# Kernel tuning notes

Hardware: AMD Instinct MI355X
Metric: run time of the kernel (lower is better)

The kernel has to match this reference:

```python
import jax, jax.numpy as jnp
import numpy as np
from jax import lax

NAG = 3          # hardcoded in the torch module (query slices, catted_torches)
B = 4096         # batch_size per agent
H = 128          # hidden_dim
HEADS = 8
AD = H // HEADS  # attend_dim
STATE, ACT, SCAN = 48, 2, 256
OUTF, HID = 10, 256
NFEAT = 32 * (SCAN - 6)  # conv output features (two VALID convs: k5 then k3)
EPS = 1e-5

def leaky(x):
    return jnp.where(x >= 0, x, 0.01 * x)

def setup_inputs() -> dict:
    key = jax.random.key(0)
    ks = iter(jax.random.split(key, 40))
    def rn(shape, scale=0.05):
        return jax.random.normal(next(ks), shape, dtype=jnp.float32) * scale
    return {
        'obs':  jax.random.normal(next(ks), (NAG * B, STATE), jnp.float32),
        'acts': jax.random.normal(next(ks), (NAG * B, ACT), jnp.float32),
        'scan': jax.random.normal(next(ks), (NAG * B, SCAN), jnp.float32),
        'conv_w1': rn((32, 1, 5)),  'conv_b1': jnp.zeros((32,), jnp.float32),
        'conv_w2': rn((32, 32, 3)), 'conv_b2': jnp.zeros((32,), jnp.float32),
        'fc_w1': rn((256, NFEAT), 0.01), 'fc_b1': jnp.zeros((256,), jnp.float32),
        'fc_w2': rn((OUTF, 256)),        'fc_b2': jnp.zeros((OUTF,), jnp.float32),
        'enc_w': rn((H, STATE + ACT + OUTF)), 'enc_b': jnp.zeros((H,), jnp.float32),
        'Wk': rn((HEADS, AD, H)),
        'Wv': rn((HEADS, AD, H)), 'bv': jnp.zeros((HEADS, AD), jnp.float32),
        'Wq': rn((NAG, HEADS, AD, H)),
        'q1_w1': rn((HID, 2 * H)), 'q1_b1': jnp.zeros((HID,), jnp.float32),
        'q1_w2': rn((HID, HID)),   'q1_b2': jnp.zeros((HID,), jnp.float32),
        'q1_w3': rn((1, HID)),     'q1_b3': jnp.zeros((1,), jnp.float32),
        'q2_w1': rn((HID, 2 * H)), 'q2_b1': jnp.zeros((HID,), jnp.float32),
        'q2_w2': rn((HID, HID)),   'q2_b2': jnp.zeros((HID,), jnp.float32),
        'q2_w3': rn((1, HID)),     'q2_b3': jnp.zeros((1,), jnp.float32),
    }

def reference(obs, acts, scan, conv_w1, conv_b1, conv_w2, conv_b2,
              fc_w1, fc_b1, fc_w2, fc_b2, enc_w, enc_b, Wk, Wv, bv, Wq,
              q1_w1, q1_b1, q1_w2, q1_b2, q1_w3, q1_b3,
              q2_w1, q2_b1, q2_w2, q2_b2, q2_w3, q2_b3):
    dn = ('NCH', 'OIH', 'NCH')
    x = scan[:, None, :]                                            # [N,1,L]
    x = lax.conv_general_dilated(x, conv_w1, (1,), 'VALID', dimension_numbers=dn)
    x = jax.nn.relu(x + conv_b1[None, :, None])
    x = lax.conv_general_dilated(x, conv_w2, (1,), 'VALID', dimension_numbers=dn)
    x = jax.nn.relu(x + conv_b2[None, :, None])
    x = x.reshape(x.shape[0], -1)                                   # [N, NFEAT]
    x = jax.nn.relu(x @ fc_w1.T + fc_b1)
    feats = x @ fc_w2.T + fc_b2                                     # [N, OUTF]

    inps = jnp.concatenate([obs, acts, feats], axis=1)
    mu, var = inps.mean(0), inps.var(0)                             # BatchNorm1d (train, no affine)
    normed = (inps - mu) / jnp.sqrt(var + EPS)
    sa = leaky(normed @ enc_w.T + enc_b).reshape(NAG, B, H)         # [ag,B,H]

    keys = jnp.einsum('gbh,ndh->ngbd', sa, Wk)                      # [hd,ag,B,ad]
    vals = leaky(jnp.einsum('gbh,ndh->ngbd', sa, Wv) + bv[:, None, None, :])
    q = jnp.einsum('gbh,gndh->gnbd', sa, Wq)                        # [ag,hd,B,ad]

    logits = jnp.einsum('gnbd,nobd->gnbo', q, keys) / np.sqrt(AD)   # [ag,hd,B,ag]
    self_mask = jnp.eye(NAG, dtype=bool)[:, None, None, :]          # exclude own agent
    logits = jnp.where(self_mask, -jnp.inf, logits)
    w = jax.nn.softmax(logits, axis=-1)
    other = jnp.einsum('gnbo,nobd->gnbd', w, vals)                  # [ag,hd,B,ad]
    other = other.transpose(0, 2, 1, 3).reshape(NAG, B, H)          # heads concatenated

    emb = jnp.concatenate([sa, other], axis=2).reshape(NAG * B, 2 * H)

    def mlp(x, w1, b1, w2, b2, w3, b3):
        x = jax.nn.relu(x @ w1.T + b1)
        x = jax.nn.relu(x @ w2.T + b2)
        return x @ w3.T + b3

    q1 = mlp(emb, q1_w1, q1_b1, q1_w2, q1_b2, q1_w3, q1_b3)
    q2 = mlp(emb, q2_w1, q2_b1, q2_w2, q2_b2, q2_w3, q2_b3)
    return (q1, q2)
```

## Files before the change

### kernel.cpp

```cpp
#include <hip/hip_runtime.h>
#include <hip/hip_bf16.h>
#include <cstdint>
#include <cstddef>

typedef unsigned short u16;
typedef __attribute__((ext_vector_type(8))) __bf16 bf16x8;
typedef __attribute__((ext_vector_type(4))) float f32x4;

__device__ __forceinline__ u16 f2b(float f) {
  __hip_bfloat16 h = __float2bfloat16(f);
  return *reinterpret_cast<u16*>(&h);
}
__device__ __forceinline__ float b2f(u16 u) {
  union { float f; uint32_t i; } x; x.i = ((uint32_t)u) << 16; return x.f;
}
__device__ __forceinline__ f32x4 mfma16(bf16x8 a, bf16x8 b, f32x4 c) {
  return __builtin_amdgcn_mfma_f32_16x16x32_bf16(a, b, c, 0, 0, 0);
}
__device__ __forceinline__ void async16(const void* g, void* l) {
  __builtin_amdgcn_global_load_lds((const __attribute__((address_space(1))) uint32_t*)g,
                                   (__attribute__((address_space(3))) uint32_t*)l, 16, 0, 0);
}

__global__ __launch_bounds__(256) void w1_perm(const float* __restrict__ w,
                                               u16* __restrict__ o) {
  __shared__ float L[8000];
  int j = blockIdx.x, tid = threadIdx.x;
  for (int i = tid; i < 8000; i += 256) L[i] = w[(size_t)j * 8000 + i];
  __syncthreads();
  for (int i = tid; i < 8000; i += 256) {
    int tt = i >> 5, c2 = i & 31;
    o[(size_t)j * 8000 + i] = f2b(L[c2 * 250 + tt]);
  }
}

struct CvtArgs {
  const float* src[7];
  u16* dst[7];
  int cum[8];
};
__global__ __launch_bounds__(256) void f2b_multi(CvtArgs a, float* stats) {
  int i = blockIdx.x * 256 + threadIdx.x;
  if (blockIdx.x == 0 && threadIdx.x < 128) stats[threadIdx.x] = 0.f;
  int seg = 0;
  #pragma unroll
  for (int s = 1; s < 7; ++s) if (i >= a.cum[s]) seg = s;
  if (i < a.cum[7]) {
    int off = i - a.cum[seg];
    a.dst[seg][off] = f2b(a.src[seg][off]);
  }
}

__global__ __launch_bounds__(256) void conv_fused(
    const float* __restrict__ scan, const float* __restrict__ cw1,
    const float* __restrict__ cb1, const float* __restrict__ cw2,
    const float* __restrict__ cb2, u16* __restrict__ x, int row0) {
  __shared__ float s[256];
  __shared__ __align__(16) u16 h1T[258 * 32];
  __shared__ __align__(16) u16 w2r[32 * 96];
  int tid = threadIdx.x;
  int lrow = blockIdx.x;
  s[tid] = scan[(size_t)(row0 + lrow) * 256 + tid];
  for (int i = tid; i < 3072; i += 256) {
    int c2 = i / 96, rem = i - c2 * 96, k = rem >> 5, c1 = rem & 31;
    w2r[i] = f2b(cw2[(c2 * 32 + c1) * 3 + k]);
  }
  if (tid < 192) h1T[252 * 32 + tid] = 0;
  __syncthreads();
  {
    int c1 = tid & 31, pb = tid >> 5;
    float w0 = cw1[c1 * 5 + 0], w1v = cw1[c1 * 5 + 1], w2v = cw1[c1 * 5 + 2],
          w3v = cw1[c1 * 5 + 3], w4v = cw1[c1 * 5 + 4];
    float bb = cb1[c1];
    int p0 = pb * 32;
    #pragma unroll 4
    for (int i = 0; i < 32; ++i) {
      int p = p0 + i;
      if (p < 252) {
        float a = bb + s[p] * w0 + s[p + 1] * w1v + s[p + 2] * w2v +
                  s[p + 3] * w3v + s[p + 4] * w4v;
        h1T[p * 32 + c1] = f2b(fmaxf(a, 0.f));
      }
    }
  }
  __syncthreads();
  int lane = tid & 63, wv = tid >> 6;
  int l15 = lane & 15, quad = lane >> 4;
  f32x4 zero = {0.f, 0.f, 0.f, 0.f};
  f32x4 acc[4][2];
  #pragma unroll
  for (int i = 0; i < 4; ++i) { acc[i][0] = zero; acc[i][1] = zero; }
  #pragma unroll
  for (int kk = 0; kk < 3; ++kk) {
    bf16x8 b0 = *(const bf16x8*)&w2r[l15 * 96 + kk * 32 + quad * 8];
    bf16x8 b1 = *(const bf16x8*)&w2r[(16 + l15) * 96 + kk * 32 + quad * 8];
    #pragma unroll
    for (int i = 0; i < 4; ++i) {
      int t = (wv * 4 + i) * 16 + l15 + kk;
      bf16x8 a = *(const bf16x8*)&h1T[t * 32 + quad * 8];
      acc[i][0] = mfma16(a, b0, acc[i][0]);
      acc[i][1] = mfma16(a, b1, acc[i][1]);
    }
  }
  float bias0 = cb2[l15], bias1 = cb2[16 + l15];
  u16* xr = x + (size_t)lrow * 8000;
  #pragma unroll
  for (int i = 0; i < 4; ++i) {
    int tb = (wv * 4 + i) * 16 + quad * 4;
    #pragma unroll
    for (int r = 0; r < 4; ++r) {
      int t = tb + r;
      if (t < 250) {
        xr[t * 32 + l15]      = f2b(fmaxf(acc[i][0][r] + bias0, 0.f));
        xr[t * 32 + 16 + l15] = f2b(fmaxf(acc[i][1][r] + bias1, 0.f));
      }
    }
  }
}

template <int MODE>
__global__ __launch_bounds__(256) void gemm_bt(
    const u16* __restrict__ A, int lda, const u16* __restrict__ W,
    const float* __restrict__ bias, float* __restrict__ outF,
    u16* __restrict__ outB, int ldo, int ksteps, int wq_sel, size_t out_zoff) {
  __shared__ __align__(16) u16 As[128 * 32];
  __shared__ __align__(16) u16 Bs[128 * 32];
  int tid = threadIdx.x;
  int m0 = blockIdx.y * 128, n0 = blockIdx.x * 128;
  if (wq_sel) W += (size_t)(blockIdx.y >> 5) * wq_sel;
  int kbase = blockIdx.z * ksteps * 32;
  if (MODE == 0) outF += (size_t)blockIdx.z * out_zoff;
  const u16* Ap = A + (size_t)m0 * lda + kbase;
  const u16* Wp = W + (size_t)n0 * lda + kbase;
  int lane = tid & 63, wv = tid >> 6;
  int l15 = lane & 15, quad = lane >> 4;
  int wm = (wv >> 1) * 64, wn = (wv & 1) * 64;
  int r0 = tid >> 2, kc = (tid & 3) * 8;
  int r1 = (tid + 256) >> 2;
  f32x4 zero = {0.f, 0.f, 0.f, 0.f};
  f32x4 acc[4][4];
  #pragma unroll
  for (int i = 0; i < 4; ++i)
    #pragma unroll
    for (int j = 0; j < 4; ++j) acc[i][j] = zero;
  for (int ks = 0; ks < ksteps; ++ks) {
    __syncthreads();
    async16(Ap + (size_t)r0 * lda + kc, &As[tid * 8]);
    async16(Wp + (size_t)r0 * lda + kc, &Bs[tid * 8]);
    async16(Ap + (size_t)r1 * lda + kc, &As[(tid + 256) * 8]);
    async16(Wp + (size_t)r1 * lda + kc, &Bs[(tid + 256) * 8]);
    __syncthreads();
    bf16x8 af[4], bfr[4];
    #pragma unroll
    for (int i = 0; i < 4; ++i)
      af[i] = *(const bf16x8*)&As[(wm + i * 16 + l15) * 32 + quad * 8];
    #pragma unroll
    for (int j = 0; j < 4; ++j)
      bfr[j] = *(const bf16x8*)&Bs[(wn + j * 16 + l15) * 32 + quad * 8];
    #pragma unroll
    for (int i = 0; i < 4; ++i)
      #pragma unroll
      for (int j = 0; j < 4; ++j) acc[i][j] = mfma16(af[i], bfr[j], acc[i][j]);
    Ap += 32; Wp += 32;
  }
  #pragma unroll
  for (int i = 0; i < 4; ++i) {
    int mb = m0 + wm + i * 16 + quad * 4;
    #pragma unroll
    for (int j = 0; j < 4; ++j) {
      int n = n0 + wn + j * 16 + l15;
      float bv_ = (MODE == 1 || MODE == 2) ? bias[n] : 0.f;
      #pragma unroll
      for (int r = 0; r < 4; ++r) {
        float v = acc[i][j][r];
        if (MODE == 0) {
          outF[(size_t)(mb + r) * ldo + n] = v;
        } else {
          v += bv_;
          if (MODE == 1) v = fmaxf(v, 0.f);
          if (MODE == 2) v = v >= 0.f ? v : 0.01f * v;
          outB[(size_t)(mb + r) * ldo + n] = f2b(v);
        }
      }
    }
  }
}

__global__ __launch_bounds__(256) void fc2_stats(
    const float* __restrict__ hparts, const float* __restrict__ b1,
    const float* __restrict__ w2, const float* __restrict__ b2,
    const float* __restrict__ obs, const float* __restrict__ acts,
    float* __restrict__ inps, float* __restrict__ stats) {
  __shared__ float hL[32 * 260];
  __shared__ float w2L[10 * 260];
  __shared__ float b1L[256];
  __shared__ float ipL[32 * 61];
  int tid = threadIdx.x, r0 = blockIdx.x * 32;
  b1L[tid] = b1[tid];
  for (int i = tid; i < 2560; i += 256) w2L[(i >> 8) * 260 + (i & 255)] = w2[i];
  for (int i = tid; i < 32 * 48; i += 256) {
    int r = i / 48, f = i - r * 48;
    ipL[r * 61 + f] = obs[(size_t)(r0 + r) * 48 + f];
  }
  if (tid < 64) {
    int r = tid >> 1, f = tid & 1;
    ipL[r * 61 + 48 + f] = acts[(size_t)(r0 + r) * 2 + f];
  }
  __syncthreads();
  const size_t HS = (size_t)12288 * 256;
  for (int i = tid; i < 32 * 256; i += 256) {
    int r = i >> 8, c = i & 255;
    size_t g = (size_t)(r0 + r) * 256 + c;
    float v = b1L[c] + hparts[g] + hparts[g + HS] + hparts[g + 2 * HS] +
              hparts[g + 3 * HS] + hparts[g + 4 * HS];
    hL[r * 260 + c] = fmaxf(v, 0.f);
  }
  __syncthreads();
  {
    int r = tid >> 3, ob = tid & 7;
    for (int o = ob; o < 10; o += 8) {
      float a = 0.f;
      #pragma unroll 8
      for (int c = 0; c < 256; ++c) a += hL[r * 260 + c] * w2L[o * 260 + c];
      ipL[r * 61 + 50 + o] = a + b2[o];
    }
  }
  __syncthreads();
  for (int i = tid; i < 32 * 60; i += 256) {
    int r = i / 60, f = i - r * 60;
    inps[(size_t)(r0 + r) * 64 + f] = ipL[r * 61 + f];
  }
  if (tid < 60) {
    float s = 0.f, s2 = 0.f;
    for (int r = 0; r < 32; ++r) {
      float v = ipL[r * 61 + tid];
      s += v; s2 += v * v;
    }
    atomicAdd(&stats[tid], s);
    atomicAdd(&stats[64 + tid], s2);
  }
}

__global__ __launch_bounds__(256) void enc_kernel(
    const float* __restrict__ inps, const float* __restrict__ stats,
    const float* __restrict__ enc_w, const float* __restrict__ enc_b,
    u16* __restrict__ sab) {
  __shared__ float ewL[128 * 61];
  __shared__ float nrm[32 * 61];
  __shared__ float ebL[128];
  __shared__ float muL[60], ivL[60];
  int tid = threadIdx.x, r0 = blockIdx.x * 32;
  if (tid < 128) ebL[tid] = enc_b[tid];
  if (tid < 60) {
    float s = stats[tid], s2 = stats[64 + tid];
    float mu = s * (1.f / 12288.f);
    float var = s2 * (1.f / 12288.f) - mu * mu;
    muL[tid] = mu;
    ivL[tid] = rsqrtf(var + 1e-5f);
  }
  for (int i = tid; i < 128 * 60; i += 256) {
    int h = i / 60, f = i - h * 60;
    ewL[h * 61 + f] = enc_w[i];
  }
  __syncthreads();
  for (int i = tid; i < 32 * 60; i += 256) {
    int r = i / 60, f = i - r * 60;
    nrm[r * 61 + f] = (inps[(size_t)(r0 + r) * 64 + f] - muL[f]) * ivL[f];
  }
  __syncthreads();
  for (int i = tid; i < 32 * 128; i += 256) {
    int r = i >> 7, h = i & 127;
    float a = ebL[h];
    #pragma unroll 4
    for (int f = 0; f < 60; ++f) a += nrm[r * 61 + f] * ewL[h * 61 + f];
    a = a >= 0.f ? a : 0.01f * a;
    sab[(size_t)(r0 + r) * 128 + h] = f2b(a);
  }
}

__global__ __launch_bounds__(128) void attn_combine(
    const u16* __restrict__ qb, const u16* __restrict__ keysb,
    const u16* __restrict__ valsb, const u16* __restrict__ sab,
    u16* __restrict__ emb) {
  __shared__ float qL[3][128], kL[3][128], vL[3][128];
  __shared__ float lg[3][8][3], wgt[3][8][3];
  int b = blockIdx.x, t = threadIdx.x;
  #pragma unroll
  for (int o = 0; o < 3; ++o) {
    size_t base = (size_t)(o * 4096 + b) * 128 + t;
    qL[o][t] = b2f(qb[base]);
    kL[o][t] = b2f(keysb[base]);
    vL[o][t] = b2f(valsb[base]);
  }
  __syncthreads();
  if (t < 72) {
    int g = t / 24, n = (t / 3) % 8, o = t % 3;
    float a = 0.f;
    #pragma unroll
    for (int d = 0; d < 16; ++d) a += qL[g][n * 16 + d] * kL[o][n * 16 + d];
    lg[g][n][o] = (o == g) ? -1e30f : a * 0.25f;
  }
  __syncthreads();
  if (t < 24) {
    int g = t / 8, n = t % 8;
    float m = fmaxf(fmaxf(lg[g][n][0], lg[g][n][1]), lg[g][n][2]);
    float e0 = expf(lg[g][n][0] - m), e1 = expf(lg[g][n][1] - m),
          e2 = expf(lg[g][n][2] - m);
    float inv = 1.f / (e0 + e1 + e2);
    wgt[g][n][0] = e0 * inv; wgt[g][n][1] = e1 * inv; wgt[g][n][2] = e2 * inv;
  }
  __syncthreads();
  int n = t >> 4, d = t & 15;
  #pragma unroll
  for (int g = 0; g < 3; ++g) {
    float o_ = wgt[g][n][0] * vL[0][n * 16 + d] +
               wgt[g][n][1] * vL[1][n * 16 + d] +
               wgt[g][n][2] * vL[2][n * 16 + d];
    size_t rbase = (size_t)(g * 4096 + b) * 256;
    emb[rbase + 128 + t] = f2b(o_);
    emb[rbase + t] = sab[(size_t)(g * 4096 + b) * 128 + t];
  }
}

__global__ __launch_bounds__(256) void final_dot(
    const u16* __restrict__ t2a, const u16* __restrict__ t2b,
    const float* __restrict__ w3a, const float* __restrict__ b3a,
    const float* __restrict__ w3b, const float* __restrict__ b3b,
    float* __restrict__ out) {
  int wv = threadIdx.x >> 6, lane = threadIdx.x & 63;
  int row = blockIdx.x * 4 + wv;
  float sa_ = 0.f, sb_ = 0.f;
  #pragma unroll
  for (int e = 0; e < 4; ++e) {
    int c = lane * 4 + e;
    sa_ += b2f(t2a[(size_t)row * 256 + c]) * w3a[c];
    sb_ += b2f(t2b[(size_t)row * 256 + c]) * w3b[c];
  }
  #pragma unroll
  for (int off = 32; off; off >>= 1) {
    sa_ += __shfl_down(sa_, off);
    sb_ += __shfl_down(sb_, off);
  }
  if (lane == 0) {
    out[row] = sa_ + b3a[0];
    out[12288 + row] = sb_ + b3b[0];
  }
}

extern "C" void kernel_launch(void* const* d_in, const int* in_sizes, int n_in,
                              void* d_out, int out_size, void* d_ws,
                              size_t ws_size, hipStream_t stream) {
  const float* obs  = (const float*)d_in[0];
  const float* acts = (const float*)d_in[1];
  const float* scan = (const float*)d_in[2];
  const float* cw1  = (const float*)d_in[3];
  const float* cb1  = (const float*)d_in[4];
  const float* cw2  = (const float*)d_in[5];
  const float* cb2  = (const float*)d_in[6];
  const float* fw1  = (const float*)d_in[7];
  const float* fb1  = (const float*)d_in[8];
  const float* fw2  = (const float*)d_in[9];
  const float* fb2  = (const float*)d_in[10];
  const float* encw = (const float*)d_in[11];
  const float* encb = (const float*)d_in[12];
  const float* Wk   = (const float*)d_in[13];
  const float* Wv   = (const float*)d_in[14];
  const float* bv   = (const float*)d_in[15];
  const float* Wq   = (const float*)d_in[16];
  const float* q1w1 = (const float*)d_in[17];
  const float* q1b1 = (const float*)d_in[18];
  const float* q1w2 = (const float*)d_in[19];
  const float* q1b2 = (const float*)d_in[20];
  const float* q1w3 = (const float*)d_in[21];
  const float* q1b3 = (const float*)d_in[22];
  const float* q2w1 = (const float*)d_in[23];
  const float* q2b1 = (const float*)d_in[24];
  const float* q2w2 = (const float*)d_in[25];
  const float* q2b2 = (const float*)d_in[26];
  const float* q2w3 = (const float*)d_in[27];
  const float* q2b3 = (const float*)d_in[28];
  float* out = (float*)d_out;
  char* ws = (char*)d_ws;
  if (ws_size < 166003712u) return;

  u16*   x     = (u16*)(ws + 0);
  u16*   w1b   = (u16*)(ws + 98304000);
  float* hpart = (float*)(ws + 102400000);
  float* stats = (float*)(ws + 165314560);
  u16*   wkb   = (u16*)(ws + 165315584);
  u16*   wvb   = (u16*)(ws + 165348352);
  u16*   wqb   = (u16*)(ws + 165381120);
  u16*   m1a   = (u16*)(ws + 165479424);
  u16*   m2a   = (u16*)(ws + 165610496);
  u16*   m1b   = (u16*)(ws + 165741568);
  u16*   m2b   = (u16*)(ws + 165872640);
  float* inps  = (float*)(ws + 0);
  u16*   sab   = (u16*)(ws + 3145728);
  u16*   keysb = (u16*)(ws + 6291456);
  u16*   valsb = (u16*)(ws + 9437184);
  u16*   qb    = (u16*)(ws + 12582912);
  u16*   embb  = (u16*)(ws + 15728640);
  u16*   t1a   = (u16*)(ws + 22020096);
  u16*   t2a   = (u16*)(ws + 28311552);
  u16*   t1b   = (u16*)(ws + 34603008);
  u16*   t2b   = (u16*)(ws + 40894464);

  w1_perm<<<256, 256, 0, stream>>>(fw1, w1b);
  CvtArgs ca;
  ca.src[0] = Wk;  ca.src[1] = Wv;  ca.src[2] = Wq;  ca.src[3] = q1w1;
  ca.src[4] = q1w2; ca.src[5] = q2w1; ca.src[6] = q2w2;
  ca.dst[0] = wkb; ca.dst[1] = wvb; ca.dst[2] = wqb; ca.dst[3] = m1a;
  ca.dst[4] = m2a; ca.dst[5] = m1b; ca.dst[6] = m2b;
  const int sz[7] = {16384, 16384, 49152, 65536, 65536, 65536, 65536};
  int cum = 0;
  ca.cum[0] = 0;
  for (int i = 0; i < 7; ++i) { cum += sz[i]; ca.cum[i + 1] = cum; }
  f2b_multi<<<1344, 256, 0, stream>>>(ca, stats);

  for (int s = 0; s < 2; ++s) {
    conv_fused<<<6144, 256, 0, stream>>>(scan, cw1, cb1, cw2, cb2, x, s * 6144);
    gemm_bt<0><<<dim3(2, 48, 5), 256, 0, stream>>>(
        x, 8000, w1b, nullptr, hpart + (size_t)s * 6144 * 256, nullptr, 256,
        50, 0, (size_t)12288 * 256);
  }
  fc2_stats<<<384, 256, 0, stream>>>(hpart, fb1, fw2, fb2, obs, acts, inps, stats);
  enc_kernel<<<384, 256, 0, stream>>>(inps, stats, encw, encb, sab);
  gemm_bt<3><<<dim3(1, 96, 1), 256, 0, stream>>>(sab, 128, wkb, nullptr, nullptr,
                                                 keysb, 128, 4, 0, 0);
  gemm_bt<2><<<dim3(1, 96, 1), 256, 0, stream>>>(sab, 128, wvb, bv, nullptr,
                                                 valsb, 128, 4, 0, 0);
  gemm_bt<3><<<dim3(1, 96, 1), 256, 0, stream>>>(sab, 128, wqb, nullptr, nullptr,
                                                 qb, 128, 4, 16384, 0);
  attn_combine<<<4096, 128, 0, stream>>>(qb, keysb, valsb, sab, embb);
  gemm_bt<1><<<dim3(2, 96, 1), 256, 0, stream>>>(embb, 256, m1a, q1b1, nullptr,
                                                 t1a, 256, 8, 0, 0);
  gemm_bt<1><<<dim3(2, 96, 1), 256, 0, stream>>>(t1a, 256, m2a, q1b2, nullptr,
                                                 t2a, 256, 8, 0, 0);
  gemm_bt<1><<<dim3(2, 96, 1), 256, 0, stream>>>(embb, 256, m1b, q2b1, nullptr,
                                                 t1b, 256, 8, 0, 0);
  gemm_bt<1><<<dim3(2, 96, 1), 256, 0, stream>>>(t1b, 256, m2b, q2b2, nullptr,
                                                 t2b, 256, 8, 0, 0);
  final_dot<<<3072, 256, 0, stream>>>(t2a, t2b, q1w3, q1b3, q2w3, q2b3, out);
}
```

Before: 444.2 us.

## Restructure conv kernel: precomputed conv2 weights, padded LDS, vectorized stores

```diff
diff --git a/kernel.cpp b/kernel.cpp
--- a/kernel.cpp
+++ b/kernel.cpp
@@ -10,6 +10,10 @@
 __device__ __forceinline__ u16 f2b(float f) {
   __hip_bfloat16 h = __float2bfloat16(f);
   return *reinterpret_cast<u16*>(&h);
+}
+__device__ __forceinline__ uint32_t pk2(float a, float b) {
+  __hip_bfloat162 h = __float22bfloat162_rn(make_float2(a, b));
+  return *reinterpret_cast<uint32_t*>(&h);
 }
 __device__ __forceinline__ float b2f(u16 u) {
   union { float f; uint32_t i; } x; x.i = ((uint32_t)u) << 16; return x.f;
@@ -35,85 +39,120 @@
 }
 
 struct CvtArgs {
-  const float* src[7];
-  u16* dst[7];
-  int cum[8];
+  const float* src[8];
+  u16* dst[8];
+  int cum[9];
 };
 __global__ __launch_bounds__(256) void f2b_multi(CvtArgs a, float* stats) {
   int i = blockIdx.x * 256 + threadIdx.x;
   if (blockIdx.x == 0 && threadIdx.x < 128) stats[threadIdx.x] = 0.f;
   int seg = 0;
   #pragma unroll
-  for (int s = 1; s < 7; ++s) if (i >= a.cum[s]) seg = s;
-  if (i < a.cum[7]) {
+  for (int s = 1; s < 8; ++s) if (i >= a.cum[s]) seg = s;
+  if (i < a.cum[8]) {
     int off = i - a.cum[seg];
-    a.dst[seg][off] = f2b(a.src[seg][off]);
+    if (seg == 7) {
+      int c2 = off / 96, rem = off - c2 * 96, kk = rem >> 5, c1 = rem & 31;
+      a.dst[7][off] = f2b(a.src[7][(c2 * 32 + c1) * 3 + kk]);
+    } else {
+      a.dst[seg][off] = f2b(a.src[seg][off]);
+    }
   }
 }
 
 __global__ __launch_bounds__(256) void conv_fused(
     const float* __restrict__ scan, const float* __restrict__ cw1,
-    const float* __restrict__ cb1, const float* __restrict__ cw2,
+    const float* __restrict__ cb1, const u16* __restrict__ w2g,
     const float* __restrict__ cb2, u16* __restrict__ x, int row0) {
-  __shared__ float s[256];
-  __shared__ __align__(16) u16 h1T[258 * 32];
-  __shared__ __align__(16) u16 w2r[32 * 96];
+  __shared__ float s[260];
+  __shared__ __align__(16) u16 h1T[258 * 40];
   int tid = threadIdx.x;
   int lrow = blockIdx.x;
-  s[tid] = scan[(size_t)(row0 + lrow) * 256 + tid];
-  for (int i = tid; i < 3072; i += 256) {
-    int c2 = i / 96, rem = i - c2 * 96, k = rem >> 5, c1 = rem & 31;
-    w2r[i] = f2b(cw2[(c2 * 32 + c1) * 3 + k]);
-  }
-  if (tid < 192) h1T[252 * 32 + tid] = 0;
-  __syncthreads();
-  {
-    int c1 = tid & 31, pb = tid >> 5;
-    float w0 = cw1[c1 * 5 + 0], w1v = cw1[c1 * 5 + 1], w2v = cw1[c1 * 5 + 2],
-          w3v = cw1[c1 * 5 + 3], w4v = cw1[c1 * 5 + 4];
-    float bb = cb1[c1];
-    int p0 = pb * 32;
-    #pragma unroll 4
-    for (int i = 0; i < 32; ++i) {
-      int p = p0 + i;
-      if (p < 252) {
-        float a = bb + s[p] * w0 + s[p + 1] * w1v + s[p + 2] * w2v +
-                  s[p + 3] * w3v + s[p + 4] * w4v;
-        h1T[p * 32 + c1] = f2b(fmaxf(a, 0.f));
-      }
-    }
-  }
-  __syncthreads();
   int lane = tid & 63, wv = tid >> 6;
   int l15 = lane & 15, quad = lane >> 4;
+  s[tid] = scan[(size_t)(row0 + lrow) * 256 + tid];
+  if (tid < 4) s[256 + tid] = 0.f;
+  if (tid < 240) h1T[252 * 40 + tid] = 0;
+  bf16x8 wfrag[2][3];
+  #pragma unroll
+  for (int i = 0; i < 2; ++i)
+    #pragma unroll
+    for (int kk = 0; kk < 3; ++kk)
+      wfrag[i][kk] = *(const bf16x8*)&w2g[(i * 16 + l15) * 96 + kk * 32 + quad * 8];
+  float bias[2][4];
+  #pragma unroll
+  for (int i = 0; i < 2; ++i)
+    #pragma unroll
+    for (int r = 0; r < 4; ++r) bias[i][r] = cb2[i * 16 + quad * 4 + r];
+  __syncthreads();
+  {
+    int cpair = tid & 15, pr = tid >> 4;
+    int c0 = cpair * 2;
+    float wA[5], wB[5];
+    #pragma unroll
+    for (int k = 0; k < 5; ++k) { wA[k] = cw1[c0 * 5 + k]; wB[k] = cw1[c0 * 5 + 5 + k]; }
+    float bA = cb1[c0], bB = cb1[c0 + 1];
+    float sv[20];
+    int p0 = pr * 16;
+    #pragma unroll
+    for (int j = 0; j < 5; ++j) {
+      f32x4 v = *(const f32x4*)&s[p0 + 4 * j];
+      sv[4 * j] = v[0]; sv[4 * j + 1] = v[1]; sv[4 * j + 2] = v[2]; sv[4 * j + 3] = v[3];
+    }
+    #pragma unroll
+    for (int ii = 0; ii < 16; ++ii) {
+      float va = bA, vb = bB;
+      #pragma unroll
+      for (int k = 0; k < 5; ++k) {
+        va += sv[ii + k] * wA[k];
+        vb += sv[ii + k] * wB[k];
+      }
+      int p = p0 + ii;
+      if (p < 252) {
+        *(uint32_t*)&h1T[p * 40 + c0] = pk2(fmaxf(va, 0.f), fmaxf(vb, 0.f));
+      }
+    }
+  }
+  __syncthreads();
   f32x4 zero = {0.f, 0.f, 0.f, 0.f};
   f32x4 acc[4][2];
   #pragma unroll
-  for (int i = 0; i < 4; ++i) { acc[i][0] = zero; acc[i][1] = zero; }
+  for (int jj = 0; jj < 4; ++jj) { acc[jj][0] = zero; acc[jj][1] = zero; }
   #pragma unroll
   for (int kk = 0; kk < 3; ++kk) {
-    bf16x8 b0 = *(const bf16x8*)&w2r[l15 * 96 + kk * 32 + quad * 8];
-    bf16x8 b1 = *(const bf16x8*)&w2r[(16 + l15) * 96 + kk * 32 + quad * 8];
-    #pragma unroll
-    for (int i = 0; i < 4; ++i) {
-      int t = (wv * 4 + i) * 16 + l15 + kk;
-      bf16x8 a = *(const bf16x8*)&h1T[t * 32 + quad * 8];
-      acc[i][0] = mfma16(a, b0, acc[i][0]);
-      acc[i][1] = mfma16(a, b1, acc[i][1]);
-    }
-  }
-  float bias0 = cb2[l15], bias1 = cb2[16 + l15];
+    #pragma unroll
+    for (int jj = 0; jj < 4; ++jj) {
+      int t = (wv * 4 + jj) * 16 + l15 + kk;
+      bf16x8 h = *(const bf16x8*)&h1T[t * 40 + quad * 8];
+      acc[jj][0] = mfma16(wfrag[0][kk], h, acc[jj][0]);
+      acc[jj][1] = mfma16(wfrag[1][kk], h, acc[jj][1]);
+    }
+  }
+  __syncthreads();
+  #pragma unroll
+  for (int jj = 0; jj < 4; ++jj) {
+    int t = (wv * 4 + jj) * 16 + l15;
+    if (t < 250) {
+      #pragma unroll
+      for (int i = 0; i < 2; ++i) {
+        float v0 = fmaxf(acc[jj][i][0] + bias[i][0], 0.f);
+        float v1 = fmaxf(acc[jj][i][1] + bias[i][1], 0.f);
+        float v2 = fmaxf(acc[jj][i][2] + bias[i][2], 0.f);
+        float v3 = fmaxf(acc[jj][i][3] + bias[i][3], 0.f);
+        uint2 pr2; pr2.x = pk2(v0, v1); pr2.y = pk2(v2, v3);
+        *(uint2*)&h1T[t * 40 + i * 16 + quad * 4] = pr2;
+      }
+    }
+  }
+  __syncthreads();
   u16* xr = x + (size_t)lrow * 8000;
   #pragma unroll
-  for (int i = 0; i < 4; ++i) {
-    int tb = (wv * 4 + i) * 16 + quad * 4;
-    #pragma unroll
-    for (int r = 0; r < 4; ++r) {
-      int t = tb + r;
-      if (t < 250) {
-        xr[t * 32 + l15]      = f2b(fmaxf(acc[i][0][r] + bias0, 0.f));
-        xr[t * 32 + 16 + l15] = f2b(fmaxf(acc[i][1][r] + bias1, 0.f));
-      }
+  for (int it = 0; it < 4; ++it) {
+    int e0 = (it * 256 + tid) * 8;
+    if (e0 < 8000) {
+      int t = e0 >> 5, c8 = (e0 >> 3) & 3;
+      bf16x8 v = *(const bf16x8*)&h1T[t * 40 + c8 * 8];
+      *(bf16x8*)&xr[e0] = v;
     }
   }
 }
@@ -381,7 +420,7 @@
   const float* q2b3 = (const float*)d_in[28];
   float* out = (float*)d_out;
   char* ws = (char*)d_ws;
-  if (ws_size < 166003712u) return;
+  if (ws_size < 166009856u) return;
 
   u16*   x     = (u16*)(ws + 0);
   u16*   w1b   = (u16*)(ws + 98304000);
@@ -394,6 +433,7 @@
   u16*   m2a   = (u16*)(ws + 165610496);
   u16*   m1b   = (u16*)(ws + 165741568);
   u16*   m2b   = (u16*)(ws + 165872640);
+  u16*   w2g   = (u16*)(ws + 166003712);
   float* inps  = (float*)(ws + 0);
   u16*   sab   = (u16*)(ws + 3145728);
   u16*   keysb = (u16*)(ws + 6291456);
@@ -408,17 +448,17 @@
   w1_perm<<<256, 256, 0, stream>>>(fw1, w1b);
   CvtArgs ca;
   ca.src[0] = Wk;  ca.src[1] = Wv;  ca.src[2] = Wq;  ca.src[3] = q1w1;
-  ca.src[4] = q1w2; ca.src[5] = q2w1; ca.src[6] = q2w2;
+  ca.src[4] = q1w2; ca.src[5] = q2w1; ca.src[6] = q2w2; ca.src[7] = cw2;
   ca.dst[0] = wkb; ca.dst[1] = wvb; ca.dst[2] = wqb; ca.dst[3] = m1a;
-  ca.dst[4] = m2a; ca.dst[5] = m1b; ca.dst[6] = m2b;
-  const int sz[7] = {16384, 16384, 49152, 65536, 65536, 65536, 65536};
+  ca.dst[4] = m2a; ca.dst[5] = m1b; ca.dst[6] = m2b; ca.dst[7] = w2g;
+  const int sz[8] = {16384, 16384, 49152, 65536, 65536, 65536, 65536, 3072};
   int cum = 0;
   ca.cum[0] = 0;
-  for (int i = 0; i < 7; ++i) { cum += sz[i]; ca.cum[i + 1] = cum; }
-  f2b_multi<<<1344, 256, 0, stream>>>(ca, stats);
+  for (int i = 0; i < 8; ++i) { cum += sz[i]; ca.cum[i + 1] = cum; }
+  f2b_multi<<<(cum + 255) / 256, 256, 0, stream>>>(ca, stats);
 
   for (int s = 0; s < 2; ++s) {
-    conv_fused<<<6144, 256, 0, stream>>>(scan, cw1, cb1, cw2, cb2, x, s * 6144);
+    conv_fused<<<6144, 256, 0, stream>>>(scan, cw1, cb1, w2g, cb2, x, s * 6144);
     gemm_bt<0><<<dim3(2, 48, 5), 256, 0, stream>>>(
         x, 8000, w1b, nullptr, hpart + (size_t)s * 6144 * 256, nullptr, 256,
         50, 0, (size_t)12288 * 256);
```

Measured after the change: 414.5 us. 6.7% less time.
